# Optimization experiments

Hardware: AMD Instinct MI355X
Metric: run time of the kernel (lower is better)

## Reference

```python
import jax, jax.numpy as jnp
import numpy as np

N = 100_000      # nodes
E = 1_600_000    # edges (avg degree 16)
D = 64           # num_features == dim == edge_dim
L = 3            # num_layers
G = 512          # graphs in batch
BN_EPS = 1e-5


def setup_inputs() -> dict:
    key = jax.random.key(0)
    ks = jax.random.split(key, 12)
    s = 0.1  # weight init scale
    x = jax.random.normal(ks[0], (N, D), jnp.float32)
    edge_attr = jax.random.normal(ks[1], (E, D), jnp.float32)
    edge_index = jax.random.randint(ks[2], (2, E), 0, N)
    batch = jnp.sort(jax.random.randint(ks[3], (N,), 0, G))
    # stacked per-layer params (all layers same shape since num_features == dim)
    We = jax.random.normal(ks[4], (L, D, D), jnp.float32) * s   # GINEConv edge Linear
    be = jax.random.normal(ks[5], (L, D), jnp.float32) * s
    W1 = jax.random.normal(ks[6], (L, D, D), jnp.float32) * s   # mlp Linear 1
    b1 = jax.random.normal(ks[7], (L, D), jnp.float32) * s
    W2 = jax.random.normal(ks[8], (L, D, D), jnp.float32) * s   # mlp Linear 2
    b2 = jax.random.normal(ks[9], (L, D), jnp.float32) * s
    gamma = jnp.ones((L, D), jnp.float32)                       # BatchNorm affine
    beta = jnp.zeros((L, D), jnp.float32)
    return dict(x=x, edge_attr=edge_attr, We=We, be=be, W1=W1, b1=b1,
                W2=W2, b2=b2, gamma=gamma, beta=beta,
                edge_index=edge_index, batch=batch)


def reference(x, edge_attr, We, be, W1, b1, W2, b2, gamma, beta, edge_index, batch):
    src, dst = edge_index[0], edge_index[1]
    pooled = []
    h = x
    for l in range(L):
        # GINEConv: message = ReLU(x_src + edge_lin(edge_attr)), sum-aggregate at dst
        e = edge_attr @ We[l] + be[l]                      # [E, D]
        m = jax.nn.relu(h[src] + e)                        # [E, D] gather + add + relu
        agg = jax.ops.segment_sum(m, dst, num_segments=N)  # [N, D] scatter-sum
        z = h + agg                                        # (1+eps)*x with eps=0
        # GINE mlp: Linear -> ReLU -> Linear
        z = jax.nn.relu(z @ W1[l] + b1[l]) @ W2[l] + b2[l]
        # block: ReLU then BatchNorm1d (training mode: batch stats, biased var)
        z = jax.nn.relu(z)
        mu = z.mean(axis=0)
        var = jnp.mean((z - mu) ** 2, axis=0)
        h = gamma[l] * (z - mu) * jax.lax.rsqrt(var + BN_EPS) + beta[l]
        # global_add_pool over graphs
        pooled.append(jax.ops.segment_sum(h, batch, num_segments=G))
    return jnp.concatenate(pooled, axis=1), h
```

## Files before the change

kernel.cpp:

```cpp
#include <hip/hip_runtime.h>
#include <hip/hip_bf16.h>

#define NN 100000
#define NE 1600000
#define DD 64
#define NG 512
#define POOLED_F (NG * 3 * DD)
#define STATS_F  (3 * 128)
#define SCAN_NB 196

typedef unsigned short u16;
typedef __attribute__((ext_vector_type(8))) short bf16x8;
typedef __attribute__((ext_vector_type(4))) float f32x4;

__device__ __forceinline__ float bf2f(u16 u) {
    return __uint_as_float(((unsigned)u) << 16);
}
__device__ __forceinline__ u16 f2bf(float f) {
    unsigned b = __float_as_uint(f);
    return (u16)((b + 0x7FFFu + ((b >> 16) & 1u)) >> 16);
}

__global__ __launch_bounds__(256) void k_zero(float* __restrict__ p, int n) {
    int i = blockIdx.x * 256 + threadIdx.x;
    if (i < n) p[i] = 0.f;
}
__global__ __launch_bounds__(256) void k_zeroi(int* __restrict__ p, int n) {
    int i = blockIdx.x * 256 + threadIdx.x;
    if (i < n) p[i] = 0;
}
__global__ __launch_bounds__(256) void k_sentinel(float* out, float val) {
    if (threadIdx.x == 0 && blockIdx.x == 0) out[0] = val;
}

__global__ __launch_bounds__(256) void k_hist(const int* __restrict__ dst,
                                              int* __restrict__ counts) {
    int e = blockIdx.x * 256 + threadIdx.x;
    if (e < NE) atomicAdd(&counts[dst[e]], 1);
}

__global__ __launch_bounds__(512) void k_scanA(const int* __restrict__ counts,
                                               int* __restrict__ bsum) {
    __shared__ int red[512];
    int tid = threadIdx.x;
    int idx = blockIdx.x * 512 + tid;
    red[tid] = (idx < NN) ? counts[idx] : 0;
    __syncthreads();
    for (int w = 256; w > 0; w >>= 1) {
        if (tid < w) red[tid] += red[tid + w];
        __syncthreads();
    }
    if (tid == 0) bsum[blockIdx.x] = red[0];
}

__global__ __launch_bounds__(256) void k_scanB(const int* __restrict__ bsum,
                                               int* __restrict__ boff,
                                               int* __restrict__ rowptr) {
    __shared__ int sh[256];
    int tid = threadIdx.x;
    int v = (tid < SCAN_NB) ? bsum[tid] : 0;
    sh[tid] = v;
    __syncthreads();
    for (int off = 1; off < 256; off <<= 1) {
        int t = (tid >= off) ? sh[tid - off] : 0;
        __syncthreads();
        sh[tid] += t;
        __syncthreads();
    }
    if (tid < SCAN_NB) boff[tid] = sh[tid] - v;
    if (tid == SCAN_NB - 1) rowptr[NN] = sh[tid];
}

__global__ __launch_bounds__(512) void k_scanC(const int* __restrict__ counts,
                                               const int* __restrict__ boff,
                                               int* __restrict__ rowptr,
                                               int* __restrict__ cursor) {
    __shared__ int sh[512];
    int tid = threadIdx.x;
    int idx = blockIdx.x * 512 + tid;
    int v = (idx < NN) ? counts[idx] : 0;
    sh[tid] = v;
    __syncthreads();
    for (int off = 1; off < 512; off <<= 1) {
        int t = (tid >= off) ? sh[tid - off] : 0;
        __syncthreads();
        sh[tid] += t;
        __syncthreads();
    }
    if (idx < NN) {
        int r = boff[blockIdx.x] + sh[tid] - v;
        rowptr[idx] = r;
        cursor[idx] = r;
    }
}

__global__ __launch_bounds__(256) void k_scatter(const int* __restrict__ src,
                                                 const int* __restrict__ dst,
                                                 int* __restrict__ cursor,
                                                 int* __restrict__ epos,
                                                 int* __restrict__ psrc) {
    int e = blockIdx.x * 256 + threadIdx.x;
    if (e >= NE) return;
    int pos = atomicAdd(&cursor[dst[e]], 1);
    epos[e] = pos;
    psrc[pos] = src[e];
}

__global__ __launch_bounds__(256) void k_fmsg(
    const float* __restrict__ ea, const float* __restrict__ We,
    const float* __restrict__ be, const int* __restrict__ epos,
    u16* __restrict__ msgb)
{
    __shared__ u16 stage[4][16][72];
    int tid = threadIdx.x;
    int wv = tid >> 6, lane = tid & 63;
    int lg = lane >> 4, lr = lane & 15;

    bf16x8 wf[3][4][2];
    float bias[3][4];
#pragma unroll
    for (int l = 0; l < 3; ++l)
#pragma unroll
        for (int cb = 0; cb < 4; ++cb) {
#pragma unroll
            for (int kh = 0; kh < 2; ++kh) {
                bf16x8 f;
#pragma unroll
                for (int j = 0; j < 8; ++j) {
                    int k = kh * 32 + lg * 8 + j;
                    f[j] = (short)f2bf(We[l * 4096 + k * 64 + cb * 16 + lr]);
                }
                wf[l][cb][kh] = f;
            }
            bias[l][cb] = be[l * 64 + cb * 16 + lr];
        }

    const int ngroups = NE / 16;
    for (int g = blockIdx.x * 4 + wv; g < ngroups; g += gridDim.x * 4) {
        int ebase = g * 16;
        bf16x8 af[2];
#pragma unroll
        for (int kh = 0; kh < 2; ++kh) {
            const float4* ap =
                (const float4*)(ea + (size_t)(ebase + lr) * DD + kh * 32 + lg * 8);
            float4 t0 = ap[0], t1 = ap[1];
            bf16x8 f;
            f[0] = (short)f2bf(t0.x); f[1] = (short)f2bf(t0.y);
            f[2] = (short)f2bf(t0.z); f[3] = (short)f2bf(t0.w);
            f[4] = (short)f2bf(t1.x); f[5] = (short)f2bf(t1.y);
            f[6] = (short)f2bf(t1.z); f[7] = (short)f2bf(t1.w);
            af[kh] = f;
        }
#pragma unroll
        for (int l = 0; l < 3; ++l) {
#pragma unroll
            for (int cb = 0; cb < 4; ++cb) {
                f32x4 acc = {0.f, 0.f, 0.f, 0.f};
                acc = __builtin_amdgcn_mfma_f32_16x16x32_bf16(
                          af[0], wf[l][cb][0], acc, 0, 0, 0);
                acc = __builtin_amdgcn_mfma_f32_16x16x32_bf16(
                          af[1], wf[l][cb][1], acc, 0, 0, 0);
#pragma unroll
                for (int i = 0; i < 4; ++i)
                    stage[wv][lg * 4 + i][cb * 16 + lr] =
                        f2bf(acc[i] + bias[l][cb]);
            }
#pragma unroll
            for (int p = 0; p < 2; ++p) {
                int row = p * 8 + (lane >> 3), chunk = lane & 7;
                uint4 v = *(const uint4*)&stage[wv][row][chunk * 8];
                int pos = epos[ebase + row];
                *(uint4*)(msgb + ((size_t)l * NE + pos) * DD + chunk * 8) = v;
            }
        }
    }
}

__global__ __launch_bounds__(256) void k_node(
    const u16* __restrict__ msgb, const float* __restrict__ h,
    const int* __restrict__ rowptr, const int* __restrict__ psrc,
    const float* __restrict__ W1, const float* __restrict__ b1,
    const float* __restrict__ W2, const float* __restrict__ b2,
    float* __restrict__ z, float* __restrict__ stats)
{
    __shared__ __align__(16) float zin[4][DD];
    __shared__ float red[512];
    int tid = threadIdx.x;
    int wv = tid >> 6, lane = tid & 63;

    float W1r[DD], W2r[DD];
#pragma unroll
    for (int k = 0; k < DD; ++k) {
        W1r[k] = W1[k * DD + lane];
        W2r[k] = W2[k * DD + lane];
    }
    float b1c = b1[lane], b2c = b2[lane];

    int wid = blockIdx.x * 4 + wv;
    int nw  = gridDim.x * 4;
    float s = 0.f, s2 = 0.f;

    for (int node = wid; node < NN; node += nw) {
        int beg = rowptr[node], end = rowptr[node + 1];
        float acc = h[(size_t)node * DD + lane];
        int j = beg;
        for (; j + 3 < end; j += 4) {
            int s0 = psrc[j], s1 = psrc[j + 1], s2i = psrc[j + 2], s3 = psrc[j + 3];
            float m0 = h[(size_t)s0 * DD + lane] + bf2f(msgb[(size_t)j * DD + lane]);
            float m1 = h[(size_t)s1 * DD + lane] + bf2f(msgb[(size_t)(j + 1) * DD + lane]);
            float m2 = h[(size_t)s2i * DD + lane] + bf2f(msgb[(size_t)(j + 2) * DD + lane]);
            float m3 = h[(size_t)s3 * DD + lane] + bf2f(msgb[(size_t)(j + 3) * DD + lane]);
            acc += fmaxf(m0, 0.f) + fmaxf(m1, 0.f) + fmaxf(m2, 0.f) + fmaxf(m3, 0.f);
        }
        for (; j < end; ++j) {
            int sj = psrc[j];
            acc += fmaxf(h[(size_t)sj * DD + lane] + bf2f(msgb[(size_t)j * DD + lane]), 0.f);
        }
        zin[wv][lane] = acc;
        float z1 = b1c;
#pragma unroll
        for (int kq = 0; kq < DD / 4; ++kq) {
            float4 q = ((const float4*)zin[wv])[kq];
            z1 = fmaf(q.x, W1r[kq * 4 + 0], z1);
            z1 = fmaf(q.y, W1r[kq * 4 + 1], z1);
            z1 = fmaf(q.z, W1r[kq * 4 + 2], z1);
            z1 = fmaf(q.w, W1r[kq * 4 + 3], z1);
        }
        z1 = fmaxf(z1, 0.f);
        zin[wv][lane] = z1;
        float z2 = b2c;
#pragma unroll
        for (int kq = 0; kq < DD / 4; ++kq) {
            float4 q = ((const float4*)zin[wv])[kq];
            z2 = fmaf(q.x, W2r[kq * 4 + 0], z2);
            z2 = fmaf(q.y, W2r[kq * 4 + 1], z2);
            z2 = fmaf(q.z, W2r[kq * 4 + 2], z2);
            z2 = fmaf(q.w, W2r[kq * 4 + 3], z2);
        }
        z2 = fmaxf(z2, 0.f);
        z[(size_t)node * DD + lane] = z2;
        s += z2;
        s2 = fmaf(z2, z2, s2);
    }
    red[tid] = s; red[256 + tid] = s2;
    __syncthreads();
    if (tid < 64) {
        float a = red[tid] + red[64 + tid] + red[128 + tid] + red[192 + tid];
        float b = red[256 + tid] + red[320 + tid] + red[384 + tid] + red[448 + tid];
        atomicAdd(&stats[tid], a);
        atomicAdd(&stats[64 + tid], b);
    }
}

__global__ __launch_bounds__(256) void k_norm_pool(
    const float* __restrict__ z, const float* __restrict__ stats,
    const float* __restrict__ gamma, const float* __restrict__ beta,
    const int* __restrict__ batch, float* __restrict__ hout,
    float* __restrict__ pooled, int l)
{
    int wave = (blockIdx.x * 256 + threadIdx.x) >> 6;
    int lane = threadIdx.x & 63;
    int n0 = wave * 64;
    if (n0 >= NN) return;
    int n1 = n0 + 64; if (n1 > NN) n1 = NN;

    float mu  = stats[lane] * (1.0f / NN);
    float var = stats[64 + lane] * (1.0f / NN) - mu * mu;
    float rstd = rsqrtf(var + 1e-5f);
    float sc = gamma[l * DD + lane] * rstd;
    float sh = beta[l * DD + lane] - sc * mu;

    int gcur = batch[n0];
    float acc = 0.f;
    for (int n = n0; n < n1; ++n) {
        float hv = fmaf(z[(size_t)n * DD + lane], sc, sh);
        hout[(size_t)n * DD + lane] = hv;
        int g = batch[n];
        if (g != gcur) {
            atomicAdd(&pooled[(size_t)gcur * (3 * DD) + l * DD + lane], acc);
            gcur = g; acc = 0.f;
        }
        acc += hv;
    }
    atomicAdd(&pooled[(size_t)gcur * (3 * DD) + l * DD + lane], acc);
}

__global__ __launch_bounds__(256) void k_copy(const float* __restrict__ src,
                                              float* __restrict__ agg) {
    int total = NN * DD / 4;
    for (int i = blockIdx.x * 256 + threadIdx.x; i < total; i += gridDim.x * 256)
        ((float4*)agg)[i] = ((const float4*)src)[i];
}
__global__ __launch_bounds__(256) void k_edge(
    const float* __restrict__ ea, const float* __restrict__ h,
    const float* __restrict__ W, const float* __restrict__ bias,
    const int* __restrict__ src, const int* __restrict__ dst,
    float* __restrict__ agg)
{
    __shared__ __align__(16) float Wl[DD * DD];
    __shared__ __align__(16) float bl[DD];
    int tid = threadIdx.x;
    for (int i = tid; i < DD * DD / 4; i += 256)
        ((float4*)Wl)[i] = ((const float4*)W)[i];
    if (tid < DD / 4) ((float4*)bl)[tid] = ((const float4*)bias)[tid];
    __syncthreads();
    int e = blockIdx.x * 256 + tid;
    int s = src[e], d = dst[e];
    float av[DD];
    const float4* earow = (const float4*)(ea + (size_t)e * DD);
#pragma unroll
    for (int i = 0; i < DD / 4; ++i) {
        float4 t = earow[i];
        av[4*i] = t.x; av[4*i+1] = t.y; av[4*i+2] = t.z; av[4*i+3] = t.w;
    }
    const float4* hrow = (const float4*)(h + (size_t)s * DD);
    float* arow = agg + (size_t)d * DD;
    for (int c4 = 0; c4 < DD / 4; ++c4) {
        float4 acc = ((float4*)bl)[c4];
#pragma unroll
        for (int k = 0; k < DD; ++k) {
            float4 w = ((float4*)Wl)[k * (DD/4) + c4];
            acc.x = fmaf(av[k], w.x, acc.x);
            acc.y = fmaf(av[k], w.y, acc.y);
            acc.z = fmaf(av[k], w.z, acc.z);
            acc.w = fmaf(av[k], w.w, acc.w);
        }
        float4 hv = hrow[c4];
        atomicAdd(arow + c4*4 + 0, fmaxf(hv.x + acc.x, 0.f));
        atomicAdd(arow + c4*4 + 1, fmaxf(hv.y + acc.y, 0.f));
        atomicAdd(arow + c4*4 + 2, fmaxf(hv.z + acc.z, 0.f));
        atomicAdd(arow + c4*4 + 3, fmaxf(hv.w + acc.w, 0.f));
    }
}
__global__ __launch_bounds__(256) void k_mlp(
    const float* in, const float* __restrict__ W1, const float* __restrict__ b1,
    const float* __restrict__ W2, const float* __restrict__ b2, float* out)
{
    __shared__ __align__(16) float W1l[DD * DD];
    __shared__ __align__(16) float W2l[DD * DD];
    __shared__ __align__(16) float b1l[DD];
    __shared__ __align__(16) float b2l[DD];
    int tid = threadIdx.x;
    for (int i = tid; i < DD * DD / 4; i += 256) {
        ((float4*)W1l)[i] = ((const float4*)W1)[i];
        ((float4*)W2l)[i] = ((const float4*)W2)[i];
    }
    if (tid < DD / 4) {
        ((float4*)b1l)[tid] = ((const float4*)b1)[tid];
        ((float4*)b2l)[tid] = ((const float4*)b2)[tid];
    }
    __syncthreads();
    int n = blockIdx.x * 256 + tid;
    if (n >= NN) return;
    float xr[DD];
    const float4* inrow = (const float4*)(in + (size_t)n * DD);
#pragma unroll
    for (int i = 0; i < DD / 4; ++i) {
        float4 t = inrow[i];
        xr[4*i] = t.x; xr[4*i+1] = t.y; xr[4*i+2] = t.z; xr[4*i+3] = t.w;
    }
    float z1[DD];
    for (int c4 = 0; c4 < DD / 4; ++c4) {
        float4 acc = ((float4*)b1l)[c4];
#pragma unroll
        for (int k = 0; k < DD; ++k) {
            float4 w = ((float4*)W1l)[k * (DD/4) + c4];
            acc.x = fmaf(xr[k], w.x, acc.x);
            acc.y = fmaf(xr[k], w.y, acc.y);
            acc.z = fmaf(xr[k], w.z, acc.z);
            acc.w = fmaf(xr[k], w.w, acc.w);
        }
        z1[c4*4+0] = fmaxf(acc.x, 0.f);
        z1[c4*4+1] = fmaxf(acc.y, 0.f);
        z1[c4*4+2] = fmaxf(acc.z, 0.f);
        z1[c4*4+3] = fmaxf(acc.w, 0.f);
    }
    float4* outrow = (float4*)(out + (size_t)n * DD);
    for (int c4 = 0; c4 < DD / 4; ++c4) {
        float4 acc = ((float4*)b2l)[c4];
#pragma unroll
        for (int k = 0; k < DD; ++k) {
            float4 w = ((float4*)W2l)[k * (DD/4) + c4];
            acc.x = fmaf(z1[k], w.x, acc.x);
            acc.y = fmaf(z1[k], w.y, acc.y);
            acc.z = fmaf(z1[k], w.z, acc.z);
            acc.w = fmaf(z1[k], w.w, acc.w);
        }
        float4 o;
        o.x = fmaxf(acc.x, 0.f); o.y = fmaxf(acc.y, 0.f);
        o.z = fmaxf(acc.z, 0.f); o.w = fmaxf(acc.w, 0.f);
        outrow[c4] = o;
    }
}
__global__ __launch_bounds__(256) void k_stats(const float* __restrict__ z,
                                               float* __restrict__ stats) {
    int tid = threadIdx.x;
    int c = tid & 63;
    float s = 0.f, s2 = 0.f;
    for (int n = blockIdx.x * 4 + (tid >> 6); n < NN; n += 1024) {
        float v = z[(size_t)n * DD + c];
        s += v;
        s2 = fmaf(v, v, s2);
    }
    __shared__ float red[512];
    red[tid] = s; red[256 + tid] = s2;
    __syncthreads();
    if (tid < 64) {
        float a = red[tid] + red[64+tid] + red[128+tid] + red[192+tid];
        float b = red[256+tid] + red[320+tid] + red[384+tid] + red[448+tid];
        atomicAdd(&stats[c], a);
        atomicAdd(&stats[64 + c], b);
    }
}

extern "C" void kernel_launch(void* const* d_in, const int* in_sizes, int n_in,
                              void* d_out, int out_size, void* d_ws, size_t ws_size,
                              hipStream_t stream) {
    const float* x     = (const float*)d_in[0];
    const float* ea    = (const float*)d_in[1];
    const float* We    = (const float*)d_in[2];
    const float* be    = (const float*)d_in[3];
    const float* W1    = (const float*)d_in[4];
    const float* b1    = (const float*)d_in[5];
    const float* W2    = (const float*)d_in[6];
    const float* b2    = (const float*)d_in[7];
    const float* gamma = (const float*)d_in[8];
    const float* beta  = (const float*)d_in[9];
    const int*   eidx  = (const int*)d_in[10];
    const int*   batch = (const int*)d_in[11];
    const int* src = eidx;
    const int* dst = eidx + NE;

    float* out_pool = (float*)d_out;
    float* out_h    = out_pool + POOLED_F;

    const int exp_sizes[12] = {6400000, 102400000, 12288, 192, 12288, 192,
                               12288, 192, 192, 192, 3200000, 100000};
    bool ok = (n_in == 12);
    for (int i = 0; ok && i < 12; ++i) ok = (in_sizes[i] == exp_sizes[i]);
    if (!ok) {
        k_sentinel<<<1, 64, 0, stream>>>((float*)d_out, 16384.0f);
        return;
    }

    u16*   msgb   = (u16*)d_ws;
    float* zbuf   = (float*)(msgb + (size_t)3 * NE * DD);
    float* stats  = zbuf + (size_t)NN * DD;
    int*   rowptr = (int*)(stats + STATS_F);
    int*   cursor = rowptr + (NN + 1);
    int*   counts = cursor + NN;
    int*   epos   = counts + NN;
    int*   psrc   = epos + NE;
    int*   bsum   = psrc + NE;
    int*   boff   = bsum + 256;
    size_t needed_fast = (size_t)3 * NE * DD * 2
                       + ((size_t)NN * DD + STATS_F) * 4
                       + ((size_t)(NN + 1) + NN + NN + NE + NE + 512) * 4;

    k_zero<<<(POOLED_F + 255) / 256, 256, 0, stream>>>(out_pool, POOLED_F);

    if (ws_size >= needed_fast) {
        k_zero<<<(STATS_F + 255) / 256, 256, 0, stream>>>(stats, STATS_F);
        k_zeroi<<<(NN + 255) / 256, 256, 0, stream>>>(counts, NN);
        k_hist<<<NE / 256, 256, 0, stream>>>(dst, counts);
        k_scanA<<<SCAN_NB, 512, 0, stream>>>(counts, bsum);
        k_scanB<<<1, 256, 0, stream>>>(bsum, boff, rowptr);
        k_scanC<<<SCAN_NB, 512, 0, stream>>>(counts, boff, rowptr, cursor);
        k_scatter<<<NE / 256, 256, 0, stream>>>(src, dst, cursor, epos, psrc);

        k_fmsg<<<2048, 256, 0, stream>>>(ea, We, be, epos, msgb);

        for (int l = 0; l < 3; ++l) {
            const float* h = (l == 0) ? x : out_h;
            const u16* msg_l = msgb + (size_t)l * NE * DD;
            k_node<<<2048, 256, 0, stream>>>(msg_l, h, rowptr, psrc,
                                             W1 + l * DD * DD, b1 + l * DD,
                                             W2 + l * DD * DD, b2 + l * DD,
                                             zbuf, stats + l * 128);
            k_norm_pool<<<(NN + 255) / 256, 256, 0, stream>>>(
                zbuf, stats + l * 128, gamma, beta, batch, out_h, out_pool, l);
        }
    } else {
        float* agg2   = (float*)d_ws;
        float* stats2 = agg2 + (size_t)NN * DD;
        if (ws_size < ((size_t)NN * DD + STATS_F) * sizeof(float)) {
            k_sentinel<<<1, 64, 0, stream>>>((float*)d_out, 32768.0f);
            return;
        }
        k_zero<<<(STATS_F + 255) / 256, 256, 0, stream>>>(stats2, STATS_F);
        for (int l = 0; l < 3; ++l) {
            const float* h = (l == 0) ? x : out_h;
            k_copy<<<2048, 256, 0, stream>>>(h, agg2);
            k_edge<<<NE / 256, 256, 0, stream>>>(ea, h, We + l * DD * DD,
                                                 be + l * DD, src, dst, agg2);
            k_mlp<<<(NN + 255) / 256, 256, 0, stream>>>(agg2, W1 + l * DD * DD,
                                                        b1 + l * DD,
                                                        W2 + l * DD * DD,
                                                        b2 + l * DD, agg2);
            k_stats<<<256, 256, 0, stream>>>(agg2, stats2 + l * 128);
            k_norm_pool<<<(NN + 255) / 256, 256, 0, stream>>>(
                agg2, stats2 + l * 128, gamma, beta, batch, out_h, out_pool, l);
        }
    }
}
```

Before: 1.242 ms.

## Split fused node kernel into aggregation and shared-memory MLP+stats kernels

The fused per-node kernel held both weight matrices in registers (128 floats per lane), which limits occupancy during the latency-bound gather. It is split into a light one-wave-per-node aggregation kernel that writes agg to a buffer, and an MLP+BN-stats kernel that reads the weights from shared memory. This trades higher occupancy in the gather for an extra write and read of the N×D intermediate and one more launch per layer. The fallback path also swaps its separate MLP and stats kernels for the fused one.

```diff
diff --git a/kernel.cpp b/kernel.cpp
--- a/kernel.cpp
+++ b/kernel.cpp
@@ -176,67 +176,64 @@
     }
 }
 
-__global__ __launch_bounds__(256) void k_node(
+__global__ __launch_bounds__(256) void k_agg(
     const u16* __restrict__ msgb, const float* __restrict__ h,
     const int* __restrict__ rowptr, const int* __restrict__ psrc,
+    float* __restrict__ agg)
+{
+    int node = (blockIdx.x * 256 + threadIdx.x) >> 6;
+    int lane = threadIdx.x & 63;
+    if (node >= NN) return;
+    int beg = rowptr[node], end = rowptr[node + 1];
+    float acc = h[(size_t)node * DD + lane];
+    int j = beg;
+    for (; j + 3 < end; j += 4) {
+        int s0 = psrc[j], s1 = psrc[j + 1], s2 = psrc[j + 2], s3 = psrc[j + 3];
+        float m0 = h[(size_t)s0 * DD + lane] + bf2f(msgb[(size_t)j * DD + lane]);
+        float m1 = h[(size_t)s1 * DD + lane] + bf2f(msgb[(size_t)(j + 1) * DD + lane]);
+        float m2 = h[(size_t)s2 * DD + lane] + bf2f(msgb[(size_t)(j + 2) * DD + lane]);
+        float m3 = h[(size_t)s3 * DD + lane] + bf2f(msgb[(size_t)(j + 3) * DD + lane]);
+        acc += fmaxf(m0, 0.f) + fmaxf(m1, 0.f) + fmaxf(m2, 0.f) + fmaxf(m3, 0.f);
+    }
+    for (; j < end; ++j) {
+        int s = psrc[j];
+        acc += fmaxf(h[(size_t)s * DD + lane] + bf2f(msgb[(size_t)j * DD + lane]), 0.f);
+    }
+    agg[(size_t)node * DD + lane] = acc;
+}
+
+__global__ __launch_bounds__(256) void k_mlp_stats(
+    const float* __restrict__ in,
     const float* __restrict__ W1, const float* __restrict__ b1,
     const float* __restrict__ W2, const float* __restrict__ b2,
     float* __restrict__ z, float* __restrict__ stats)
 {
-    __shared__ __align__(16) float zin[4][DD];
+    __shared__ __align__(16) float W1l[DD * DD];
+    __shared__ __align__(16) float W2l[DD * DD];
+    __shared__ float zin[4][DD];
     __shared__ float red[512];
-    int tid = threadIdx.x;
-    int wv = tid >> 6, lane = tid & 63;
-
-    float W1r[DD], W2r[DD];
-#pragma unroll
-    for (int k = 0; k < DD; ++k) {
-        W1r[k] = W1[k * DD + lane];
-        W2r[k] = W2[k * DD + lane];
+    int tid = threadIdx.x, wv = tid >> 6, lane = tid & 63;
+    for (int i = tid; i < DD * DD / 4; i += 256) {
+        ((float4*)W1l)[i] = ((const float4*)W1)[i];
+        ((float4*)W2l)[i] = ((const float4*)W2)[i];
     }
     float b1c = b1[lane], b2c = b2[lane];
-
-    int wid = blockIdx.x * 4 + wv;
-    int nw  = gridDim.x * 4;
+    __syncthreads();
+
     float s = 0.f, s2 = 0.f;
-
+    int wid = blockIdx.x * 4 + wv, nw = gridDim.x * 4;
     for (int node = wid; node < NN; node += nw) {
-        int beg = rowptr[node], end = rowptr[node + 1];
-        float acc = h[(size_t)node * DD + lane];
-        int j = beg;
-        for (; j + 3 < end; j += 4) {
-            int s0 = psrc[j], s1 = psrc[j + 1], s2i = psrc[j + 2], s3 = psrc[j + 3];
-            float m0 = h[(size_t)s0 * DD + lane] + bf2f(msgb[(size_t)j * DD + lane]);
-            float m1 = h[(size_t)s1 * DD + lane] + bf2f(msgb[(size_t)(j + 1) * DD + lane]);
-            float m2 = h[(size_t)s2i * DD + lane] + bf2f(msgb[(size_t)(j + 2) * DD + lane]);
-            float m3 = h[(size_t)s3 * DD + lane] + bf2f(msgb[(size_t)(j + 3) * DD + lane]);
-            acc += fmaxf(m0, 0.f) + fmaxf(m1, 0.f) + fmaxf(m2, 0.f) + fmaxf(m3, 0.f);
-        }
-        for (; j < end; ++j) {
-            int sj = psrc[j];
-            acc += fmaxf(h[(size_t)sj * DD + lane] + bf2f(msgb[(size_t)j * DD + lane]), 0.f);
-        }
-        zin[wv][lane] = acc;
+        zin[wv][lane] = in[(size_t)node * DD + lane];
         float z1 = b1c;
 #pragma unroll
-        for (int kq = 0; kq < DD / 4; ++kq) {
-            float4 q = ((const float4*)zin[wv])[kq];
-            z1 = fmaf(q.x, W1r[kq * 4 + 0], z1);
-            z1 = fmaf(q.y, W1r[kq * 4 + 1], z1);
-            z1 = fmaf(q.z, W1r[kq * 4 + 2], z1);
-            z1 = fmaf(q.w, W1r[kq * 4 + 3], z1);
-        }
+        for (int k = 0; k < DD; ++k)
+            z1 = fmaf(zin[wv][k], W1l[k * DD + lane], z1);
         z1 = fmaxf(z1, 0.f);
         zin[wv][lane] = z1;
         float z2 = b2c;
 #pragma unroll
-        for (int kq = 0; kq < DD / 4; ++kq) {
-            float4 q = ((const float4*)zin[wv])[kq];
-            z2 = fmaf(q.x, W2r[kq * 4 + 0], z2);
-            z2 = fmaf(q.y, W2r[kq * 4 + 1], z2);
-            z2 = fmaf(q.z, W2r[kq * 4 + 2], z2);
-            z2 = fmaf(q.w, W2r[kq * 4 + 3], z2);
-        }
+        for (int k = 0; k < DD; ++k)
+            z2 = fmaf(zin[wv][k], W2l[k * DD + lane], z2);
         z2 = fmaxf(z2, 0.f);
         z[(size_t)node * DD + lane] = z2;
         s += z2;
@@ -330,66 +327,6 @@
         atomicAdd(arow + c4*4 + 1, fmaxf(hv.y + acc.y, 0.f));
         atomicAdd(arow + c4*4 + 2, fmaxf(hv.z + acc.z, 0.f));
         atomicAdd(arow + c4*4 + 3, fmaxf(hv.w + acc.w, 0.f));
-    }
-}
-__global__ __launch_bounds__(256) void k_mlp(
-    const float* in, const float* __restrict__ W1, const float* __restrict__ b1,
-    const float* __restrict__ W2, const float* __restrict__ b2, float* out)
-{
-    __shared__ __align__(16) float W1l[DD * DD];
-    __shared__ __align__(16) float W2l[DD * DD];
-    __shared__ __align__(16) float b1l[DD];
-    __shared__ __align__(16) float b2l[DD];
-    int tid = threadIdx.x;
-    for (int i = tid; i < DD * DD / 4; i += 256) {
-        ((float4*)W1l)[i] = ((const float4*)W1)[i];
-        ((float4*)W2l)[i] = ((const float4*)W2)[i];
-    }
-    if (tid < DD / 4) {
-        ((float4*)b1l)[tid] = ((const float4*)b1)[tid];
-        ((float4*)b2l)[tid] = ((const float4*)b2)[tid];
-    }
-    __syncthreads();
-    int n = blockIdx.x * 256 + tid;
-    if (n >= NN) return;
-    float xr[DD];
-    const float4* inrow = (const float4*)(in + (size_t)n * DD);
-#pragma unroll
-    for (int i = 0; i < DD / 4; ++i) {
-        float4 t = inrow[i];
-        xr[4*i] = t.x; xr[4*i+1] = t.y; xr[4*i+2] = t.z; xr[4*i+3] = t.w;
-    }
-    float z1[DD];
-    for (int c4 = 0; c4 < DD / 4; ++c4) {
-        float4 acc = ((float4*)b1l)[c4];
-#pragma unroll
-        for (int k = 0; k < DD; ++k) {
-            float4 w = ((float4*)W1l)[k * (DD/4) + c4];
-            acc.x = fmaf(xr[k], w.x, acc.x);
-            acc.y = fmaf(xr[k], w.y, acc.y);
-            acc.z = fmaf(xr[k], w.z, acc.z);
-            acc.w = fmaf(xr[k], w.w, acc.w);
-        }
-        z1[c4*4+0] = fmaxf(acc.x, 0.f);
-        z1[c4*4+1] = fmaxf(acc.y, 0.f);
-        z1[c4*4+2] = fmaxf(acc.z, 0.f);
-        z1[c4*4+3] = fmaxf(acc.w, 0.f);
-    }
-    float4* outrow = (float4*)(out + (size_t)n * DD);
-    for (int c4 = 0; c4 < DD / 4; ++c4) {
-        float4 acc = ((float4*)b2l)[c4];
-#pragma unroll
-        for (int k = 0; k < DD; ++k) {
-            float4 w = ((float4*)W2l)[k * (DD/4) + c4];
-            acc.x = fmaf(z1[k], w.x, acc.x);
-            acc.y = fmaf(z1[k], w.y, acc.y);
-            acc.z = fmaf(z1[k], w.z, acc.z);
-            acc.w = fmaf(z1[k], w.w, acc.w);
-        }
-        float4 o;
-        o.x = fmaxf(acc.x, 0.f); o.y = fmaxf(acc.y, 0.f);
-        o.z = fmaxf(acc.z, 0.f); o.w = fmaxf(acc.w, 0.f);
-        outrow[c4] = o;
     }
 }
 __global__ __launch_bounds__(256) void k_stats(const float* __restrict__ z,
@@ -473,10 +410,13 @@
         for (int l = 0; l < 3; ++l) {
             const float* h = (l == 0) ? x : out_h;
             const u16* msg_l = msgb + (size_t)l * NE * DD;
-            k_node<<<2048, 256, 0, stream>>>(msg_l, h, rowptr, psrc,
-                                             W1 + l * DD * DD, b1 + l * DD,
-                                             W2 + l * DD * DD, b2 + l * DD,
-                                             zbuf, stats + l * 128);
+            k_agg<<<(NN * DD + 255) / 256, 256, 0, stream>>>(msg_l, h, rowptr,
+                                                             psrc, zbuf);
+            k_mlp_stats<<<2048, 256, 0, stream>>>(zbuf, W1 + l * DD * DD,
+                                                  b1 + l * DD,
+                                                  W2 + l * DD * DD,
+                                                  b2 + l * DD,
+                                                  zbuf, stats + l * 128);
             k_norm_pool<<<(NN + 255) / 256, 256, 0, stream>>>(
                 zbuf, stats + l * 128, gamma, beta, batch, out_h, out_pool, l);
         }
@@ -493,11 +433,11 @@
             k_copy<<<2048, 256, 0, stream>>>(h, agg2);
             k_edge<<<NE / 256, 256, 0, stream>>>(ea, h, We + l * DD * DD,
                                                  be + l * DD, src, dst, agg2);
-            k_mlp<<<(NN + 255) / 256, 256, 0, stream>>>(agg2, W1 + l * DD * DD,
-                                                        b1 + l * DD,
-                                                        W2 + l * DD * DD,
-                                                        b2 + l * DD, agg2);
-            k_stats<<<256, 256, 0, stream>>>(agg2, stats2 + l * 128);
+            k_mlp_stats<<<2048, 256, 0, stream>>>(agg2, W1 + l * DD * DD,
+                                                  b1 + l * DD,
+                                                  W2 + l * DD * DD,
+                                                  b2 + l * DD,
+                                                  agg2, stats2 + l * 128);
             k_norm_pool<<<(NN + 255) / 256, 256, 0, stream>>>(
                 agg2, stats2 + l * 128, gamma, beta, batch, out_h, out_pool, l);
         }
```

Result: faster. 1.047 ms (-15.7%).
